# Performance work log

Measured on AMD Instinct MI355X. Metric: run time of the kernel, lower is better.

The kernel has to match this reference:

```python
import jax, jax.numpy as jnp
import numpy as np

ALPHA = 0.2  # LeakyReLU negative slope


def setup_inputs() -> dict:
    key = jax.random.key(0)
    k1, k2, k3, k4 = jax.random.split(key, 4)
    N, E, F_IN, F_OUT = 100000, 1600000, 128, 32
    x = jax.random.normal(k1, (N, F_IN), dtype=jnp.float32)
    W = jax.random.normal(k2, (F_IN, F_OUT), dtype=jnp.float32) * 0.1
    a = jax.random.normal(k3, (2 * F_OUT, 1), dtype=jnp.float32) * 0.1
    edge_index = jax.random.randint(k4, (2, E), 0, N, dtype=jnp.int64)
    return {"x": x, "W": W, "a": a, "edge_index": edge_index}


def reference(x, W, a, edge_index):
    N = x.shape[0]
    F_OUT = W.shape[1]
    Wx = x @ W  # [N, F_OUT]
    src = edge_index[0]  # row indices (softmax groups)
    dst = edge_index[1]
    # e = leakyrelu([Wx_i || Wx_j] @ a); split a to avoid materializing the concat
    a_src = a[:F_OUT, 0]
    a_dst = a[F_OUT:, 0]
    e = (Wx @ a_src)[src] + (Wx @ a_dst)[dst]  # [E]
    e = jnp.where(e >= 0, e, ALPHA * e)
    # sparse softmax over rows (src)
    m = jax.ops.segment_max(e, src, num_segments=N)  # -inf for empty rows
    m = jnp.where(jnp.isinf(m), 0.0, m)
    exp_v = jnp.exp(e - m[src])
    s = jax.ops.segment_sum(exp_v, src, num_segments=N)
    s = jnp.where(s == 0, 1.0, s)
    att = exp_v / s[src]  # [E]
    # sparse matmul: h[i] = sum_j att[i,j] * Wx[j]
    h = jax.ops.segment_sum(att[:, None] * Wx[dst], src, num_segments=N)
    return jax.nn.elu(h)
```

## Files before the change

kernel.cpp:

```cpp
#include <hip/hip_runtime.h>
#include <hip/hip_bf16.h>
#include <math.h>

#define ALPHA 0.2f
#define F_IN 128
#define F_OUT 32
#define BSHIFT 7
#define BNODES 128
#define DSTBITS 17
#define CHUNK 8192
#define SLABCAP 3072
#define NBKMAX 800
#define MAXPER 6
#define CURSTRIDE 16

typedef __attribute__((ext_vector_type(8))) short short8;
typedef __attribute__((ext_vector_type(4))) float float4v;

__device__ __forceinline__ short f2bf(float f) {
    __hip_bfloat16 h = __float2bfloat16(f);
    return __builtin_bit_cast(short, h);
}
__device__ __forceinline__ float bf_lo(unsigned u) {
    return __uint_as_float(u << 16);
}
__device__ __forceinline__ float bf_hi(unsigned u) {
    return __uint_as_float(u & 0xFFFF0000u);
}

__global__ __launch_bounds__(512) void k_phaseA(
    const float* __restrict__ x, const float* __restrict__ W,
    const float* __restrict__ a, unsigned short* __restrict__ Wxh,
    float* __restrict__ s1, float* __restrict__ s2, int nTiles, int N, int nT1,
    const int* __restrict__ src, const int* __restrict__ dst,
    int* __restrict__ bcur, unsigned* __restrict__ packed, int E, int NBK)
{
    if ((int)blockIdx.x < nT1) {
        __shared__ short Wt[32 * 136];
        for (int i = threadIdx.x; i < F_IN * F_OUT; i += 512) {
            int k = i >> 5, n = i & 31;
            Wt[n * 136 + k] = f2bf(W[i]);
        }
        __syncthreads();

        int wave = threadIdx.x >> 6;
        int lane = threadIdx.x & 63;
        int tile = blockIdx.x * 8 + wave;
        if (tile >= nTiles) return;

        int m    = lane & 15;
        int quad = lane >> 4;
        int row  = tile * 16 + m;
        int rowc = row < N ? row : N - 1;

        short8 bf[2][4];
#pragma unroll
        for (int t = 0; t < 2; ++t)
#pragma unroll
            for (int s = 0; s < 4; ++s)
                bf[t][s] = *(const short8*)&Wt[(t * 16 + m) * 136 + s * 32 + quad * 8];

        float4v acc0 = {0.f, 0.f, 0.f, 0.f};
        float4v acc1 = {0.f, 0.f, 0.f, 0.f};
        const float* xr = x + (size_t)rowc * F_IN + quad * 8;
#pragma unroll
        for (int s = 0; s < 4; ++s) {
            float4 xa = *(const float4*)(xr + s * 32);
            float4 xb = *(const float4*)(xr + s * 32 + 4);
            short8 af;
            af[0] = f2bf(xa.x); af[1] = f2bf(xa.y); af[2] = f2bf(xa.z); af[3] = f2bf(xa.w);
            af[4] = f2bf(xb.x); af[5] = f2bf(xb.y); af[6] = f2bf(xb.z); af[7] = f2bf(xb.w);
            acc0 = __builtin_amdgcn_mfma_f32_16x16x32_bf16(af, bf[0][s], acc0, 0, 0, 0);
            acc1 = __builtin_amdgcn_mfma_f32_16x16x32_bf16(af, bf[1][s], acc1, 0, 0, 0);
        }

        int rbase = tile * 16 + quad * 4;
#pragma unroll
        for (int r = 0; r < 4; ++r) {
            if (rbase + r < N) {
                Wxh[(size_t)(rbase + r) * F_OUT + m]      = (unsigned short)f2bf(acc0[r]);
                Wxh[(size_t)(rbase + r) * F_OUT + m + 16] = (unsigned short)f2bf(acc1[r]);
            }
        }

        float a1c0 = a[m], a1c1 = a[m + 16];
        float a2c0 = a[F_OUT + m], a2c1 = a[F_OUT + m + 16];
#pragma unroll
        for (int r = 0; r < 4; ++r) {
            float v1 = acc0[r] * a1c0 + acc1[r] * a1c1;
            float v2 = acc0[r] * a2c0 + acc1[r] * a2c1;
#pragma unroll
            for (int off = 8; off >= 1; off >>= 1) {
                v1 += __shfl_xor(v1, off, 16);
                v2 += __shfl_xor(v2, off, 16);
            }
            if (m == 0 && rbase + r < N) {
                s1[rbase + r] = v1;
                s2[rbase + r] = v2;
            }
        }
    } else {
        __shared__ int hist[NBKMAX];
        __shared__ int cur[NBKMAX];
        int t = threadIdx.x;
        for (int i = t; i < NBK; i += 512) hist[i] = 0;
        __syncthreads();
        int e0 = ((int)blockIdx.x - nT1) * CHUNK;
        int sreg[16], dreg[16];
#pragma unroll
        for (int k = 0; k < 4; ++k) {
            int e = e0 + k * 2048 + t * 4;
            int4 s4, d4;
            if (e + 3 < E) {
                s4 = *(const int4*)&src[e];
                d4 = *(const int4*)&dst[e];
            } else {
                s4.x = (e + 0 < E) ? src[e + 0] : -1;
                s4.y = (e + 1 < E) ? src[e + 1] : -1;
                s4.z = (e + 2 < E) ? src[e + 2] : -1;
                s4.w = (e + 3 < E) ? src[e + 3] : -1;
                d4.x = (e + 0 < E) ? dst[e + 0] : 0;
                d4.y = (e + 1 < E) ? dst[e + 1] : 0;
                d4.z = (e + 2 < E) ? dst[e + 2] : 0;
                d4.w = (e + 3 < E) ? dst[e + 3] : 0;
            }
            sreg[k * 4 + 0] = s4.x; dreg[k * 4 + 0] = d4.x;
            sreg[k * 4 + 1] = s4.y; dreg[k * 4 + 1] = d4.y;
            sreg[k * 4 + 2] = s4.z; dreg[k * 4 + 2] = d4.z;
            sreg[k * 4 + 3] = s4.w; dreg[k * 4 + 3] = d4.w;
        }
#pragma unroll
        for (int k = 0; k < 16; ++k)
            if (sreg[k] >= 0) atomicAdd(&hist[sreg[k] >> BSHIFT], 1);
        __syncthreads();
        for (int i = t; i < NBK; i += 512)
            if (hist[i] > 0) cur[i] = atomicAdd(&bcur[i * CURSTRIDE], hist[i]);
        __syncthreads();
#pragma unroll
        for (int k = 0; k < 16; ++k) {
            if (sreg[k] >= 0) {
                int b = sreg[k] >> BSHIFT;
                int p = atomicAdd(&cur[b], 1);
                if (p < SLABCAP)
                    packed[(size_t)b * SLABCAP + p] =
                        ((unsigned)(sreg[k] & (BNODES - 1)) << DSTBITS) | (unsigned)dreg[k];
            }
        }
    }
}

__global__ __launch_bounds__(512) void k_bnode(
    const unsigned* __restrict__ packed, const int* __restrict__ bcur,
    const float* __restrict__ s1, const float* __restrict__ s2,
    const unsigned short* __restrict__ Wxh, float* __restrict__ out, int N)
{
    __shared__ unsigned sorted[SLABCAP];
    __shared__ int psum[BNODES];
    __shared__ int rpl[BNODES];
    __shared__ int degl[BNODES];
    __shared__ int cur[BNODES];
    __shared__ int histl[BNODES];
    __shared__ float s1l[BNODES];

    int b = blockIdx.x;
    int t = threadIdx.x;
    int n0 = b << BSHIFT;
    int cnt = min(bcur[b * CURSTRIDE], SLABCAP);
    const unsigned* pb = packed + (size_t)b * SLABCAP;

    if (t < BNODES) {
        histl[t] = 0;
        int n = n0 + t;
        s1l[t] = (n < N) ? s1[n] : 0.f;
    }
    __syncthreads();

    unsigned ereg[MAXPER];
#pragma unroll
    for (int k = 0; k < MAXPER; ++k) {
        int j = k * 512 + t;
        ereg[k] = (j < cnt) ? pb[j] : 0xFFFFFFFFu;
    }
#pragma unroll
    for (int k = 0; k < MAXPER; ++k)
        if (ereg[k] != 0xFFFFFFFFu) atomicAdd(&histl[ereg[k] >> DSTBITS], 1);
    __syncthreads();

    int a0 = 0;
    if (t < BNODES) { a0 = histl[t]; psum[t] = a0; }
    __syncthreads();
    for (int off = 1; off < BNODES; off <<= 1) {
        int v = 0;
        if (t < BNODES && t >= off) v = psum[t - off];
        __syncthreads();
        if (t < BNODES) psum[t] += v;
        __syncthreads();
    }
    if (t < BNODES) {
        int excl = (t > 0) ? psum[t - 1] : 0;
        rpl[t] = excl;
        cur[t] = excl;
        degl[t] = a0;
    }
    __syncthreads();

#pragma unroll
    for (int k = 0; k < MAXPER; ++k) {
        if (ereg[k] != 0xFFFFFFFFu) {
            int ls = ereg[k] >> DSTBITS;
            int p = atomicAdd(&cur[ls], 1);
            sorted[p] = ereg[k];
        }
    }
    __syncthreads();

    int g = t >> 5;
    int l = t & 31;
    int es = l >> 2;
    int fq = l & 3;

    for (int ni = 0; ni < 8; ++ni) {
        int ls = g * 8 + ni;
        int n = n0 + ls;
        if (n >= N) break;
        int base = rpl[ls];
        int deg  = degl[ls];
        float s1n = s1l[ls];

        float acc[8];
#pragma unroll
        for (int c = 0; c < 8; ++c) acc[c] = 0.f;
        float sum = 0.f;

        for (int j0 = 0; j0 < deg; j0 += 32) {
            int j = j0 + l;
            int   d_l = 0;
            float p_l = 0.f;
            if (j < deg) {
                d_l = (int)(sorted[base + j] & ((1u << DSTBITS) - 1));
                float ev = s1n + s2[d_l];
                ev = ev >= 0.f ? ev : ALPHA * ev;
                p_l = __expf(ev);
            }
            sum += p_l;
            int cnt2 = min(32, deg - j0);
            int nIter = (cnt2 + 7) >> 3;
            for (int it = 0; it < nIter; ++it) {
                int e = it * 8 + es;
                float p = __shfl(p_l, e, 32);
                int   d = __shfl(d_l, e, 32);
                uint4 w = *(const uint4*)&Wxh[(size_t)d * F_OUT + fq * 8];
                acc[0] += p * bf_lo(w.x);
                acc[1] += p * bf_hi(w.x);
                acc[2] += p * bf_lo(w.y);
                acc[3] += p * bf_hi(w.y);
                acc[4] += p * bf_lo(w.z);
                acc[5] += p * bf_hi(w.z);
                acc[6] += p * bf_lo(w.w);
                acc[7] += p * bf_hi(w.w);
            }
        }
#pragma unroll
        for (int off = 4; off <= 16; off <<= 1)
#pragma unroll
            for (int c = 0; c < 8; ++c)
                acc[c] += __shfl_xor(acc[c], off, 32);
#pragma unroll
        for (int off = 16; off >= 1; off >>= 1)
            sum += __shfl_xor(sum, off, 32);

        if (es == 0) {
            float inv = (deg > 0) ? 1.f / sum : 0.f;
            float4 h0, h1;
            h0.x = acc[0] * inv; h0.y = acc[1] * inv; h0.z = acc[2] * inv; h0.w = acc[3] * inv;
            h1.x = acc[4] * inv; h1.y = acc[5] * inv; h1.z = acc[6] * inv; h1.w = acc[7] * inv;
            h0.x = h0.x > 0.f ? h0.x : expm1f(h0.x);
            h0.y = h0.y > 0.f ? h0.y : expm1f(h0.y);
            h0.z = h0.z > 0.f ? h0.z : expm1f(h0.z);
            h0.w = h0.w > 0.f ? h0.w : expm1f(h0.w);
            h1.x = h1.x > 0.f ? h1.x : expm1f(h1.x);
            h1.y = h1.y > 0.f ? h1.y : expm1f(h1.y);
            h1.z = h1.z > 0.f ? h1.z : expm1f(h1.z);
            h1.w = h1.w > 0.f ? h1.w : expm1f(h1.w);
            float* op = &out[(size_t)n * F_OUT + fq * 8];
            *(float4*)op       = h0;
            *(float4*)(op + 4) = h1;
        }
    }
}

extern "C" void kernel_launch(void* const* d_in, const int* in_sizes, int n_in,
                              void* d_out, int out_size, void* d_ws, size_t ws_size,
                              hipStream_t stream)
{
    const float* x = (const float*)d_in[0];
    const float* W = (const float*)d_in[1];
    const float* a = (const float*)d_in[2];
    const int*  ei = (const int*)d_in[3];

    int N = in_sizes[0] / F_IN;
    int E = in_sizes[3] / 2;
    const int* src = ei;
    const int* dst = ei + E;
    int NBK = (N + BNODES - 1) >> BSHIFT;
    int nTiles = (N + 15) / 16;
    int nT1 = (nTiles + 7) / 8;
    int nEB = (E + CHUNK - 1) / CHUNK;

    unsigned short* Wxh = (unsigned short*)d_ws;
    float*    s1       = (float*)d_ws + (size_t)16 * N;
    float*    s2       = s1 + N;
    int*      bcur     = (int*)(s2 + N);
    unsigned* packed   = (unsigned*)(bcur + NBKMAX * CURSTRIDE);

    float* out = (float*)d_out;

    hipMemsetAsync(bcur, 0, (size_t)NBKMAX * CURSTRIDE * 4, stream);

    k_phaseA<<<nT1 + nEB, 512, 0, stream>>>(x, W, a, Wxh, s1, s2, nTiles, N, nT1,
                                            src, dst, bcur, packed, E, NBK);
    k_bnode<<<NBK, 512, 0, stream>>>(packed, bcur, s1, s2, Wxh, out, N);
}
```

Baseline: 155.7 us.

## Use wave-shuffle scan, 8-lane feature split, and batched staged epilogue in bnode

The block-level shared-memory prefix sum over 128 nodes, which needed many barriers, becomes a single-wavefront shuffle scan over two halves. The gather loop now splits each 32-lane group into 8 feature lanes by 4 edges instead of 4 by 8. Each lane loads 8 bytes of bf16 features and keeps 4 accumulators, which lowers register pressure and shortens the cross-lane reduction. Per-node results are staged in shared memory so the normalise, ELU and store epilogue runs once for all 8 nodes of a group, using all lanes. In exchange, the edge loop runs twice as many iterations per node, the kernel uses more shared memory, and the epilogue switches to approximate rcp/exp math.

```diff
diff --git a/kernel.cpp b/kernel.cpp
--- a/kernel.cpp
+++ b/kernel.cpp
@@ -155,12 +155,13 @@
     const unsigned short* __restrict__ Wxh, float* __restrict__ out, int N)
 {
     __shared__ unsigned sorted[SLABCAP];
-    __shared__ int psum[BNODES];
     __shared__ int rpl[BNODES];
     __shared__ int degl[BNODES];
     __shared__ int cur[BNODES];
     __shared__ int histl[BNODES];
     __shared__ float s1l[BNODES];
+    __shared__ float stageL[16][8][32];
+    __shared__ float sumsL[16][8];
 
     int b = blockIdx.x;
     int t = threadIdx.x;
@@ -186,21 +187,18 @@
         if (ereg[k] != 0xFFFFFFFFu) atomicAdd(&histl[ereg[k] >> DSTBITS], 1);
     __syncthreads();
 
-    int a0 = 0;
-    if (t < BNODES) { a0 = histl[t]; psum[t] = a0; }
-    __syncthreads();
-    for (int off = 1; off < BNODES; off <<= 1) {
-        int v = 0;
-        if (t < BNODES && t >= off) v = psum[t - off];
-        __syncthreads();
-        if (t < BNODES) psum[t] += v;
-        __syncthreads();
-    }
-    if (t < BNODES) {
-        int excl = (t > 0) ? psum[t - 1] : 0;
-        rpl[t] = excl;
-        cur[t] = excl;
-        degl[t] = a0;
+    if (t < 64) {
+        int aLo = histl[t], aHi = histl[t + 64];
+        int sLo = aLo, sHi = aHi;
+#pragma unroll
+        for (int off = 1; off < 64; off <<= 1) {
+            int vLo = __shfl_up(sLo, off, 64);
+            int vHi = __shfl_up(sHi, off, 64);
+            if (t >= off) { sLo += vLo; sHi += vHi; }
+        }
+        sHi += __shfl(sLo, 63, 64);
+        rpl[t]      = sLo - aLo;  cur[t]      = sLo - aLo;  degl[t]      = aLo;
+        rpl[t + 64] = sHi - aHi;  cur[t + 64] = sHi - aHi;  degl[t + 64] = aHi;
     }
     __syncthreads();
 
@@ -216,20 +214,20 @@
 
     int g = t >> 5;
     int l = t & 31;
-    int es = l >> 2;
-    int fq = l & 3;
+    int es = l >> 3;
+    int fq = l & 7;
 
     for (int ni = 0; ni < 8; ++ni) {
-        int ls = g * 8 + ni;
+        int ls = (g << 3) + ni;
         int n = n0 + ls;
         if (n >= N) break;
         int base = rpl[ls];
         int deg  = degl[ls];
         float s1n = s1l[ls];
 
-        float acc[8];
-#pragma unroll
-        for (int c = 0; c < 8; ++c) acc[c] = 0.f;
+        float acc[4];
+#pragma unroll
+        for (int c = 0; c < 4; ++c) acc[c] = 0.f;
         float sum = 0.f;
 
         for (int j0 = 0; j0 < deg; j0 += 32) {
@@ -244,45 +242,57 @@
             }
             sum += p_l;
             int cnt2 = min(32, deg - j0);
-            int nIter = (cnt2 + 7) >> 3;
+            int nIter = (cnt2 + 3) >> 2;
             for (int it = 0; it < nIter; ++it) {
-                int e = it * 8 + es;
+                int e = (it << 2) + es;
                 float p = __shfl(p_l, e, 32);
                 int   d = __shfl(d_l, e, 32);
-                uint4 w = *(const uint4*)&Wxh[(size_t)d * F_OUT + fq * 8];
+                uint2 w = *(const uint2*)&Wxh[(size_t)d * F_OUT + fq * 4];
                 acc[0] += p * bf_lo(w.x);
                 acc[1] += p * bf_hi(w.x);
                 acc[2] += p * bf_lo(w.y);
                 acc[3] += p * bf_hi(w.y);
-                acc[4] += p * bf_lo(w.z);
-                acc[5] += p * bf_hi(w.z);
-                acc[6] += p * bf_lo(w.w);
-                acc[7] += p * bf_hi(w.w);
-            }
-        }
-#pragma unroll
-        for (int off = 4; off <= 16; off <<= 1)
-#pragma unroll
-            for (int c = 0; c < 8; ++c)
+            }
+        }
+#pragma unroll
+        for (int off = 8; off <= 16; off <<= 1)
+#pragma unroll
+            for (int c = 0; c < 4; ++c)
                 acc[c] += __shfl_xor(acc[c], off, 32);
 #pragma unroll
         for (int off = 16; off >= 1; off >>= 1)
             sum += __shfl_xor(sum, off, 32);
 
-        if (es == 0) {
-            float inv = (deg > 0) ? 1.f / sum : 0.f;
-            float4 h0, h1;
-            h0.x = acc[0] * inv; h0.y = acc[1] * inv; h0.z = acc[2] * inv; h0.w = acc[3] * inv;
-            h1.x = acc[4] * inv; h1.y = acc[5] * inv; h1.z = acc[6] * inv; h1.w = acc[7] * inv;
-            h0.x = h0.x > 0.f ? h0.x : expm1f(h0.x);
-            h0.y = h0.y > 0.f ? h0.y : expm1f(h0.y);
-            h0.z = h0.z > 0.f ? h0.z : expm1f(h0.z);
-            h0.w = h0.w > 0.f ? h0.w : expm1f(h0.w);
-            h1.x = h1.x > 0.f ? h1.x : expm1f(h1.x);
-            h1.y = h1.y > 0.f ? h1.y : expm1f(h1.y);
-            h1.z = h1.z > 0.f ? h1.z : expm1f(h1.z);
-            h1.w = h1.w > 0.f ? h1.w : expm1f(h1.w);
-            float* op = &out[(size_t)n * F_OUT + fq * 8];
+        if (l < 8) {
+            float4 v;
+            v.x = acc[0]; v.y = acc[1]; v.z = acc[2]; v.w = acc[3];
+            *(float4*)&stageL[g][ni][l * 4] = v;
+        }
+        if (l == 0)
+            sumsL[g][ni] = sum;
+    }
+
+    {
+        int ln = l >> 2;
+        int fo = (l & 3) * 8;
+        int n = n0 + (g << 3) + ln;
+        if (n < N) {
+            float s = sumsL[g][ln];
+            float inv = (s > 0.f) ? __builtin_amdgcn_rcpf(s) : 0.f;
+            const float* sp = &stageL[g][ln][fo];
+            float4 h0 = *(const float4*)sp;
+            float4 h1 = *(const float4*)(sp + 4);
+            h0.x *= inv; h0.y *= inv; h0.z *= inv; h0.w *= inv;
+            h1.x *= inv; h1.y *= inv; h1.z *= inv; h1.w *= inv;
+            h0.x = h0.x > 0.f ? h0.x : __expf(h0.x) - 1.f;
+            h0.y = h0.y > 0.f ? h0.y : __expf(h0.y) - 1.f;
+            h0.z = h0.z > 0.f ? h0.z : __expf(h0.z) - 1.f;
+            h0.w = h0.w > 0.f ? h0.w : __expf(h0.w) - 1.f;
+            h1.x = h1.x > 0.f ? h1.x : __expf(h1.x) - 1.f;
+            h1.y = h1.y > 0.f ? h1.y : __expf(h1.y) - 1.f;
+            h1.z = h1.z > 0.f ? h1.z : __expf(h1.z) - 1.f;
+            h1.w = h1.w > 0.f ? h1.w : __expf(h1.w) - 1.f;
+            float* op = &out[(size_t)n * F_OUT + fo];
             *(float4*)op       = h0;
             *(float4*)(op + 4) = h1;
         }
```

Measured after the change: 149.1 us. -4.2%, faster.
